# Kernel tuning notes

Measured on AMD Instinct MI355X. Metric: run time of the kernel, lower is better.

## Reference

```python
import jax, jax.numpy as jnp
import numpy as np

HEADS = 24
HEAD_DIM = 96
SPARSE_N = 4
ROPE_BASE = 10000.0


def _rope_cos_sin(pos, D):
    # pos: [L] int positions; D: per-axis rotary dim (even)
    inv_freq = 1.0 / (ROPE_BASE ** (jnp.arange(0, D, 2, dtype=jnp.float32) / D))
    f = pos.astype(jnp.float32)[:, None] * inv_freq[None, :]   # [L, D/2] (interp scale = 1)
    f = jnp.concatenate([f, f], axis=-1)                        # [L, D]
    return jnp.cos(f), jnp.sin(f)


def _rotate_half(x):
    x1, x2 = jnp.split(x, 2, axis=-1)
    return jnp.concatenate([-x2, x1], axis=-1)


def _apply_rope3d(tok, frame, height, width):
    # tok: [b, h, s, d]; RoPE3D splits head_dim into 3 equal chunks for (t, y, x)
    D = tok.shape[-1] // 3
    t = jnp.repeat(jnp.arange(frame), height * width)
    y = jnp.tile(jnp.repeat(jnp.arange(height), width), frame)
    x = jnp.tile(jnp.arange(width), frame * height)
    outs = []
    for i, pos in enumerate((t, y, x)):
        cos, sin = _rope_cos_sin(pos, D)                        # [s, D]
        part = tok[..., i * D:(i + 1) * D]
        outs.append(part * cos[None, None] + _rotate_half(part) * sin[None, None])
    return jnp.concatenate(outs, axis=-1)


def _sparse_1d(x, n):
    # 'b h (g k) d -> (k b) h g d' with pad so s % n*n == 0
    b, h, s, d = x.shape
    pad = (-s) % (n * n)
    if pad:
        x = jnp.pad(x, ((0, 0), (0, 0), (0, pad), (0, 0)))
    g = (s + pad) // n
    x = x.reshape(b, h, g, n, d)
    return jnp.transpose(x, (3, 0, 1, 2, 4)).reshape(n * b, h, g, d), pad


def _reverse_sparse_1d(x, n, s):
    # '(k b) h g d -> b h (g k) d' then crop to s tokens
    kb, h, g, d = x.shape
    b = kb // n
    x = x.reshape(n, b, h, g, d)
    x = jnp.transpose(x, (1, 2, 3, 0, 4)).reshape(b, h, g * n, d)
    return x[:, :, :s, :]


def setup_inputs() -> dict:
    key = jax.random.key(0)
    ks = jax.random.split(key, 5)
    dim = HEADS * HEAD_DIM
    b, f, hh, ww = 1, 8, 16, 32
    s = f * hh * ww
    inp = {
        "hidden_states": jax.random.normal(ks[0], (b, s, dim), dtype=jnp.float32),
        "wq": jax.random.normal(ks[1], (dim, dim), dtype=jnp.float32) * 0.02,
        "bq": jnp.zeros((dim,), jnp.float32),
        "wk": jax.random.normal(ks[2], (dim, dim), dtype=jnp.float32) * 0.02,
        "bk": jnp.zeros((dim,), jnp.float32),
        "wv": jax.random.normal(ks[3], (dim, dim), dtype=jnp.float32) * 0.02,
        "bv": jnp.zeros((dim,), jnp.float32),
        "wo": jax.random.normal(ks[4], (dim, dim), dtype=jnp.float32) * 0.02,
        "bo": jnp.zeros((dim,), jnp.float32),
        "frame": f, "height": hh, "width": ww,
    }
    return inp


def reference(hidden_states, wq, bq, wk, bk, wv, bv, wo, bo, frame, height, width):
    b, s, dim = hidden_states.shape
    assert s == frame * height * width

    def proj(w, bias):
        y = hidden_states @ w + bias                            # [b, s, dim]
        return jnp.transpose(y.reshape(b, s, HEADS, HEAD_DIM), (0, 2, 1, 3))  # [b, h, s, d]

    q = proj(wq, bq)
    k = proj(wk, bk)
    v = proj(wv, bv)

    # 3D rotary embedding on q, k (self-attention path)
    q = _apply_rope3d(q, frame, height, width)
    k = _apply_rope3d(k, frame, height, width)

    # sparse-1d grouping (sparse_group=False): strided token groups of size s/sparse_n
    q, _ = _sparse_1d(q, SPARSE_N)
    k, _ = _sparse_1d(k, SPARSE_N)
    v, _ = _sparse_1d(v, SPARSE_N)

    scale = 1.0 / jnp.sqrt(jnp.asarray(HEAD_DIM, jnp.float32))
    scores = jnp.einsum('bhqd,bhkd->bhqk', q, k) * scale        # [(n b), h, g, g]
    probs = jax.nn.softmax(scores, axis=-1)
    out = jnp.einsum('bhqk,bhkd->bhqd', probs, v)

    out = _reverse_sparse_1d(out, SPARSE_N, s)                   # [b, h, s, d]
    out = jnp.transpose(out, (0, 2, 1, 3)).reshape(b, s, dim)
    return out @ wo + bo
```

## Files before the change

### kernel.cpp

```cpp
#include <hip/hip_runtime.h>
#include <stdint.h>

#define S_TOK 4096
#define DIM   2304
#define NH    24
#define DH    96
#define GQ    1024
#define KDIM  2304

typedef unsigned short ushort_t;
typedef __attribute__((ext_vector_type(8))) short bf16x8;
typedef __attribute__((ext_vector_type(4))) float f32x4;

__device__ __forceinline__ ushort_t f2bf(float x) {
    union { float f; uint32_t u; } c; c.f = x;
    uint32_t u = c.u + 0x7FFFu + ((c.u >> 16) & 1u);
    return (ushort_t)(u >> 16);
}

#define GLDS(gp, lp) __builtin_amdgcn_global_load_lds( \
    (const __attribute__((address_space(1))) void*)(gp), \
    (__attribute__((address_space(3))) void*)(lp), 16, 0, 0)

__global__ __launch_bounds__(256) void cast_bf16_kernel(const float* __restrict__ in,
                                                        ushort_t* __restrict__ out, int n4) {
    int i = blockIdx.x * 256 + threadIdx.x;
    if (i >= n4) return;
    float4 v = ((const float4*)in)[i];
    ushort4 o;
    o.x = f2bf(v.x); o.y = f2bf(v.y); o.z = f2bf(v.z); o.w = f2bf(v.w);
    ((ushort4*)out)[i] = o;
}

__global__ __launch_bounds__(256) void wtrans_kernel(const float* __restrict__ W0,
                                                     const float* __restrict__ W1,
                                                     const float* __restrict__ W2,
                                                     const float* __restrict__ W3,
                                                     ushort_t* __restrict__ WT0, int dim) {
    __shared__ float tile[32][33];
    const int z = blockIdx.z;
    const float* W = (z == 0) ? W0 : (z == 1) ? W1 : (z == 2) ? W2 : W3;
    ushort_t* WT = WT0 + (size_t)z * dim * dim;
    const int bx = blockIdx.x * 32;
    const int by = blockIdx.y * 32;
    const int tx = threadIdx.x & 31, ty = threadIdx.x >> 5;
#pragma unroll
    for (int i = 0; i < 4; ++i)
        tile[ty + i*8][tx] = W[(size_t)(by + ty + i*8) * dim + bx + tx];
    __syncthreads();
#pragma unroll
    for (int i = 0; i < 4; ++i)
        WT[(size_t)(bx + ty + i*8) * dim + by + tx] = f2bf(tile[tx][ty + i*8]);
}

template<bool FINAL>
__global__ __launch_bounds__(512, 2) void gemm256(const ushort_t* __restrict__ A,
                                                  const ushort_t* __restrict__ Bt,
                                                  const float* __restrict__ bq,
                                                  const float* __restrict__ bk,
                                                  const float* __restrict__ bv,
                                                  ushort_t* __restrict__ Qb,
                                                  ushort_t* __restrict__ Kb,
                                                  ushort_t* __restrict__ Vtb,
                                                  float* __restrict__ Cf) {
    constexpr int K  = KDIM;
    constexpr int NT = K / 32;
    __shared__ ushort_t a_s[4 * 8192];
    __shared__ ushort_t b_s[4 * 8192];
    const int t = threadIdx.x, l = t & 63, w = t >> 6;
    const int wr = w >> 2, wc = w & 3, g = l >> 4, ln = l & 15;
    const int nwg = gridDim.x * gridDim.y;
    const int lin = blockIdx.y * gridDim.x + blockIdx.x;
    const int cpx = nwg >> 3;
    const int swz = (lin & 7) * cpx + (lin >> 3);
    const int bx = swz % gridDim.x, by = swz / gridDim.x;
    const int m0 = by * 256, n0 = bx * 256;

    const int swz_rd = (g ^ ((ln >> 1) & 3)) * 8;
    const int kc_src = (((t & 3) ^ ((t >> 3) & 3)) * 8);
    const int srow   = t >> 2;

    auto stageA = [&](int kt) {
        const int slot = kt & 3;
#pragma unroll
        for (int q = 0; q < 2; ++q)
            GLDS(A + (size_t)(m0 + q*128 + srow) * K + kt*32 + kc_src,
                 &a_s[slot*8192 + (q*512 + t) * 8]);
    };
    auto stageB = [&](int kt) {
        const int slot = kt & 3;
#pragma unroll
        for (int q = 0; q < 2; ++q)
            GLDS(Bt + (size_t)(n0 + q*128 + srow) * K + kt*32 + kc_src,
                 &b_s[slot*8192 + (q*512 + t) * 8]);
    };

    f32x4 acc[8][4] = {};

    stageA(0); stageB(0); stageA(1); stageB(1); stageA(2); stageB(2);
    asm volatile("s_waitcnt vmcnt(8)" ::: "memory");
    __builtin_amdgcn_s_barrier();

    for (int kt = 0; kt < NT; ++kt) {
        const int slot = kt & 3;
        bf16x8 bv4[4];
        {
            bf16x8 av[4];
#pragma unroll
            for (int j = 0; j < 4; ++j)
                bv4[j] = *(const bf16x8*)&b_s[slot*8192 + (wc*64 + j*16 + ln)*32 + swz_rd];
#pragma unroll
            for (int i = 0; i < 4; ++i)
                av[i] = *(const bf16x8*)&a_s[slot*8192 + (wr*128 + i*16 + ln)*32 + swz_rd];
            if (kt < NT - 3) stageA(kt + 3);
            __builtin_amdgcn_s_barrier();
            asm volatile("s_waitcnt lgkmcnt(0)" ::: "memory");
            __builtin_amdgcn_sched_barrier(0);
            __builtin_amdgcn_s_setprio(1);
#pragma unroll
            for (int i = 0; i < 4; ++i)
#pragma unroll
                for (int j = 0; j < 4; ++j)
                    acc[i][j] = __builtin_amdgcn_mfma_f32_16x16x32_bf16(av[i], bv4[j], acc[i][j], 0, 0, 0);
            __builtin_amdgcn_s_setprio(0);
        }
        {
            bf16x8 av[4];
#pragma unroll
            for (int i = 0; i < 4; ++i)
                av[i] = *(const bf16x8*)&a_s[slot*8192 + (wr*128 + 64 + i*16 + ln)*32 + swz_rd];
            if (kt < NT - 3) stageB(kt + 3);
            if (kt <= NT - 4)      asm volatile("s_waitcnt vmcnt(8)" ::: "memory");
            else if (kt == NT - 3) asm volatile("s_waitcnt vmcnt(4)" ::: "memory");
            else                   asm volatile("s_waitcnt vmcnt(0)" ::: "memory");
            __builtin_amdgcn_s_barrier();
            asm volatile("s_waitcnt lgkmcnt(0)" ::: "memory");
            __builtin_amdgcn_sched_barrier(0);
            __builtin_amdgcn_s_setprio(1);
#pragma unroll
            for (int i = 0; i < 4; ++i)
#pragma unroll
                for (int j = 0; j < 4; ++j)
                    acc[4 + i][j] = __builtin_amdgcn_mfma_f32_16x16x32_bf16(av[i], bv4[j], acc[4 + i][j], 0, 0, 0);
            __builtin_amdgcn_s_setprio(0);
        }
    }

    if constexpr (FINAL) {
        const float* bias = bq;
#pragma unroll
        for (int i = 0; i < 8; ++i) {
            int mb = m0 + wr*128 + i*16 + g*4;
#pragma unroll
            for (int j = 0; j < 4; ++j) {
                int n = n0 + wc*64 + j*16 + ln;
                float bb = bias[n];
#pragma unroll
                for (int r = 0; r < 4; ++r)
                    Cf[(size_t)(mb + r) * DIM + n] = acc[i][j][r] + bb;
            }
        }
    } else {
        const int mode = bx / 9;
        const int nb = (bx - mode * 9) * 256;
        const float* bias = (mode == 0) ? bq : (mode == 1) ? bk : bv;
        if (mode == 2) {
#pragma unroll
            for (int i = 0; i < 8; ++i) {
                int mb = m0 + wr*128 + i*16 + g*4;
                int q  = mb >> 2;
#pragma unroll
                for (int j = 0; j < 4; ++j) {
                    int nm = nb + wc*64 + j*16 + ln;
                    int hh = nm / DH, d = nm - hh * DH;
                    float bb = bias[nm];
#pragma unroll
                    for (int r = 0; r < 4; ++r)
                        Vtb[(size_t)(r * NH + hh) * (DH * GQ) + (size_t)d * GQ + q] =
                            f2bf(acc[i][j][r] + bb);
                }
            }
        } else {
            ushort_t* O = (mode == 0) ? Qb : Kb;
            const float scq = (mode == 0) ? 0.1020620726159658f : 1.0f;
#pragma unroll
            for (int i = 0; i < 8; ++i) {
                int mb = m0 + wr*128 + i*16 + g*4;
#pragma unroll
                for (int jp = 0; jp < 2; ++jp) {
                    int j  = jp * 2;
                    int n1 = nb + wc*64 + j*16 + ln;
                    int hh = n1 / DH, d1 = n1 - hh * DH;
                    int sec = d1 >> 5, f = d1 & 15;
                    float invf = __expf((float)f * -0.5756462732485114f);
                    float b1 = bias[n1], b2 = bias[n1 + 16];
#pragma unroll
                    for (int r = 0; r < 4; ++r) {
                        int m = mb + r;
                        int pos = (sec == 0) ? (m >> 9) : (sec == 1) ? ((m >> 5) & 15) : (m & 31);
                        float ang = (float)pos * invf;
                        float sn, cs;
                        __sincosf(ang, &sn, &cs);
                        float v1 = acc[i][j][r]     + b1;
                        float v2 = acc[i][j + 1][r] + b2;
                        size_t base = ((size_t)((m & 3) * NH + hh)) * (GQ * DH) + (size_t)(m >> 2) * DH;
                        O[base + d1]      = f2bf((v1 * cs - v2 * sn) * scq);
                        O[base + d1 + 16] = f2bf((v2 * cs + v1 * sn) * scq);
                    }
                }
            }
        }
    }
}

__global__ __launch_bounds__(256) void gemm128(const ushort_t* __restrict__ A,
                                               const ushort_t* __restrict__ Bt,
                                               const float* __restrict__ bias,
                                               float* __restrict__ C) {
    constexpr int K = KDIM;
    __shared__ ushort_t a_s[128 * 32];
    __shared__ ushort_t b_s[128 * 32];
    const int t = threadIdx.x;
    const int l = t & 63, w = t >> 6;
    const int wr = w >> 1, wc = w & 1;
    const int g = l >> 4, ln = l & 15;
    const int lin = blockIdx.y * gridDim.x + blockIdx.x;
    const int swz = (lin & 7) * 72 + (lin >> 3);
    const int bx = swz % 18, by = swz / 18;
    const int m0 = by * 128, n0 = bx * 128;

    const int swz_rd = (g ^ ((ln >> 1) & 3)) * 8;
    const int kc_src = (((t & 3) ^ ((t >> 3) & 3)) * 8);
    const int srow   = t >> 2;

    const ushort_t* Ab = A  + (size_t)(m0 + srow) * K + kc_src;
    const ushort_t* Bb = Bt + (size_t)(n0 + srow) * K + kc_src;
    ushort_t* a_d0 = a_s + t * 8;
    ushort_t* a_d1 = a_s + 2048 + t * 8;
    ushort_t* b_d0 = b_s + t * 8;
    ushort_t* b_d1 = b_s + 2048 + t * 8;
    const size_t rstep = (size_t)64 * K;

    f32x4 acc[4][4] = {};

    for (int k0 = 0; k0 < K; k0 += 32) {
        __syncthreads();
        GLDS(Ab + k0,         a_d0);
        GLDS(Ab + rstep + k0, a_d1);
        GLDS(Bb + k0,         b_d0);
        GLDS(Bb + rstep + k0, b_d1);
        __syncthreads();
        bf16x8 av[4], bv[4];
#pragma unroll
        for (int i = 0; i < 4; ++i)
            av[i] = *(const bf16x8*)&a_s[(wr*64 + i*16 + ln) * 32 + swz_rd];
#pragma unroll
        for (int j = 0; j < 4; ++j)
            bv[j] = *(const bf16x8*)&b_s[(wc*64 + j*16 + ln) * 32 + swz_rd];
#pragma unroll
        for (int i = 0; i < 4; ++i)
#pragma unroll
            for (int j = 0; j < 4; ++j)
                acc[i][j] = __builtin_amdgcn_mfma_f32_16x16x32_bf16(av[i], bv[j], acc[i][j], 0, 0, 0);
    }

#pragma unroll
    for (int i = 0; i < 4; ++i) {
        int mb = m0 + wr*64 + i*16 + g*4;
#pragma unroll
        for (int j = 0; j < 4; ++j) {
            int n = n0 + wc*64 + j*16 + ln;
            float bb = bias[n];
#pragma unroll
            for (int r = 0; r < 4; ++r)
                C[(size_t)(mb + r) * DIM + n] = acc[i][j][r] + bb;
        }
    }
}

__global__ __launch_bounds__(256, 3) void attn_kernel(const ushort_t* __restrict__ Qb,
                                                      const ushort_t* __restrict__ Kb,
                                                      const ushort_t* __restrict__ Vt,
                                                      ushort_t* __restrict__ ATT) {
    __shared__ ushort_t k_s[2][12 * 64 * 8];
    __shared__ ushort_t v_s[8 * 96 * 8];
    __shared__ ushort_t p_s[4 * 2 * 16 * 64];

    const int t = threadIdx.x, l = t & 63, w = t >> 6, g = l >> 4, ln = l & 15;
    const int lin  = blockIdx.x;
    const int swz  = (lin & 7) * 96 + (lin >> 3);
    const int inst = swz >> 3;
    const int qb0  = (swz & 7) * 128;
    const int n_idx = inst / NH, h = inst - n_idx * NH;
    const int swzp = (ln & 7) << 3;

    const ushort_t* Qi = Qb + (size_t)inst * (GQ * DH);
    const ushort_t* Ki = Kb + (size_t)inst * (GQ * DH);
    const ushort_t* Vi = Vt + (size_t)inst * (DH * GQ);

    auto stageK = [&](int kt, int b) {
#pragma unroll
        for (int it = 0; it < 3; ++it) {
            int P = t + it * 256;
            int c = P >> 6, key = P & 63;
            GLDS(Ki + (size_t)(kt * 64 + key) * DH + c * 8, &k_s[b][P * 8]);
        }
    };
    auto stageV = [&](int kt) {
#pragma unroll
        for (int it = 0; it < 3; ++it) {
            int P = t + it * 256;
            int c = P / 96, d = P - c * 96;
            GLDS(Vi + (size_t)d * GQ + kt * 64 + c * 8, &v_s[P * 8]);
        }
    };

    bf16x8 qf[2][3];
#pragma unroll
    for (int qt = 0; qt < 2; ++qt)
#pragma unroll
        for (int ks = 0; ks < 3; ++ks)
            qf[qt][ks] = *(const bf16x8*)(Qi + (size_t)(qb0 + w*32 + qt*16 + ln) * DH + ks*32 + g*8);

    float m_run[2], l_run[2];
#pragma unroll
    for (int qt = 0; qt < 2; ++qt) { m_run[qt] = -3.0e38f; l_run[qt] = 0.f; }
    f32x4 acc_o[2][6] = {};

    stageK(0, 0);
    stageV(0);
    __syncthreads();

    int cur = 0;
    for (int kt = 0; kt < 16; ++kt) {
        stageK((kt + 1) & 15, cur ^ 1);
        float al2[2];

        f32x4 sc[2][4] = {};
#pragma unroll
        for (int ct = 0; ct < 4; ++ct) {
            bf16x8 kf0 = *(const bf16x8*)&k_s[cur][((0*4 + g)*64 + ct*16 + ln) * 8];
            bf16x8 kf1 = *(const bf16x8*)&k_s[cur][((1*4 + g)*64 + ct*16 + ln) * 8];
            bf16x8 kf2 = *(const bf16x8*)&k_s[cur][((2*4 + g)*64 + ct*16 + ln) * 8];
#pragma unroll
            for (int qi = 0; qi < 2; ++qi) {
                sc[qi][ct] = __builtin_amdgcn_mfma_f32_16x16x32_bf16(kf0, qf[qi][0], sc[qi][ct], 0, 0, 0);
                sc[qi][ct] = __builtin_amdgcn_mfma_f32_16x16x32_bf16(kf1, qf[qi][1], sc[qi][ct], 0, 0, 0);
                sc[qi][ct] = __builtin_amdgcn_mfma_f32_16x16x32_bf16(kf2, qf[qi][2], sc[qi][ct], 0, 0, 0);
            }
        }
#pragma unroll
        for (int qi = 0; qi < 2; ++qi) {
            const int qt = qi;
            float mx = sc[qi][0][0];
#pragma unroll
            for (int ct = 0; ct < 4; ++ct)
#pragma unroll
                for (int r = 0; r < 4; ++r)
                    mx = fmaxf(mx, sc[qi][ct][r]);
            mx = fmaxf(mx, __shfl_xor(mx, 16, 64));
            mx = fmaxf(mx, __shfl_xor(mx, 32, 64));
            float mn = fmaxf(m_run[qt], mx);
            float al = __expf(m_run[qt] - mn);
            m_run[qt] = mn;
            float rs = 0.f;
            ushort_t pb[16];
#pragma unroll
            for (int ct = 0; ct < 4; ++ct)
#pragma unroll
                for (int r = 0; r < 4; ++r) {
                    float p = __expf(sc[qi][ct][r] - mn);
                    rs += p;
                    pb[ct*4 + r] = f2bf(p);
                }
            rs += __shfl_xor(rs, 16, 64);
            rs += __shfl_xor(rs, 32, 64);
            l_run[qt] = l_run[qt] * al + rs;
            al2[qt] = al;
            const int pbase = ((w*2 + qt)*16 + ln) * 64;
#pragma unroll
            for (int ct = 0; ct < 4; ++ct) {
                ushort4 pk;
                pk.x = pb[ct*4+0]; pk.y = pb[ct*4+1]; pk.z = pb[ct*4+2]; pk.w = pb[ct*4+3];
                *(ushort4*)&p_s[pbase + ((ct*16 + g*4) ^ swzp)] = pk;
            }
        }

#pragma unroll
        for (int qt = 0; qt < 2; ++qt)
#pragma unroll
            for (int r = 0; r < 4; ++r) {
                float a = __shfl(al2[qt], g*4 + r, 16);
#pragma unroll
                for (int dt = 0; dt < 6; ++dt)
                    acc_o[qt][dt][r] *= a;
            }

        asm volatile("s_waitcnt vmcnt(3)" ::: "memory");
        __builtin_amdgcn_s_barrier();
        __builtin_amdgcn_sched_barrier(0);
        asm volatile("s_waitcnt lgkmcnt(0)" ::: "memory");
        __builtin_amdgcn_sched_barrier(0);

#pragma unroll
        for (int kb = 0; kb < 2; ++kb) {
            bf16x8 pf2[2];
#pragma unroll
            for (int qt = 0; qt < 2; ++qt)
                pf2[qt] = *(const bf16x8*)&p_s[((w*2 + qt)*16 + ln)*64 + ((kb*32 + g*8) ^ swzp)];
#pragma unroll
            for (int dt = 0; dt < 6; ++dt) {
                bf16x8 vf = *(const bf16x8*)&v_s[((kb*4 + g)*96 + dt*16 + ln) * 8];
#pragma unroll
                for (int qt = 0; qt < 2; ++qt)
                    acc_o[qt][dt] = __builtin_amdgcn_mfma_f32_16x16x32_bf16(pf2[qt], vf, acc_o[qt][dt], 0, 0, 0);
            }
        }

        __syncthreads();
        if (kt < 15) stageV(kt + 1);
        cur ^= 1;
    }

#pragma unroll
    for (int qt = 0; qt < 2; ++qt) {
        float inv = 1.0f / l_run[qt];
#pragma unroll
        for (int r = 0; r < 4; ++r) {
            float iv = __shfl(inv, g*4 + r, 16);
            int gq = qb0 + w*32 + qt*16 + g*4 + r;
            size_t base = ((size_t)(gq * 4 + n_idx)) * DIM + h * DH;
#pragma unroll
            for (int dt = 0; dt < 6; ++dt)
                ATT[base + dt*16 + ln] = f2bf(acc_o[qt][dt][r] * iv);
        }
    }
}

extern "C" void kernel_launch(void* const* d_in, const int* in_sizes, int n_in,
                              void* d_out, int out_size, void* d_ws, size_t ws_size,
                              hipStream_t stream) {
    const float* hidden = (const float*)d_in[0];
    const float* wq = (const float*)d_in[1];
    const float* bq = (const float*)d_in[2];
    const float* wk = (const float*)d_in[3];
    const float* bk = (const float*)d_in[4];
    const float* wv = (const float*)d_in[5];
    const float* bv = (const float*)d_in[6];
    const float* wo = (const float*)d_in[7];
    const float* bo = (const float*)d_in[8];
    float* out = (float*)d_out;

    char* ws = (char*)d_ws;
    ushort_t* Xb  = (ushort_t*)ws;
    ushort_t* WTq = (ushort_t*)(ws + 18874368);
    ushort_t* WTk = WTq + (size_t)DIM * DIM;
    ushort_t* WTv = WTk + (size_t)DIM * DIM;
    ushort_t* WTo = WTv + (size_t)DIM * DIM;
    ushort_t* Qb  = WTo + (size_t)DIM * DIM;
    ushort_t* Kb  = Qb + (size_t)S_TOK * DIM;
    ushort_t* Vtb = Kb + (size_t)S_TOK * DIM;
    ushort_t* ATT = Vtb + (size_t)S_TOK * DIM;

    cast_bf16_kernel<<<dim3(9216), dim3(256), 0, stream>>>(hidden, Xb, (S_TOK * DIM) / 4);

    wtrans_kernel<<<dim3(72, 72, 4), 256, 0, stream>>>(wq, wk, wv, wo, WTq, DIM);

    gemm256<false><<<dim3(27, 16), 512, 0, stream>>>(Xb, WTq, bq, bk, bv, Qb, Kb, Vtb, nullptr);

    attn_kernel<<<dim3(768), 256, 0, stream>>>(Qb, Kb, Vtb, ATT);

    gemm128<<<dim3(18, 32), 256, 0, stream>>>(ATT, WTo, bo, out);
}
```

Measured before the change: 328.0 us.

## Double-buffer LDS in output-projection GEMM with prefetch-two-ahead pipeline

Converts the gemm128 main loop from a single LDS buffer with two barriers per k-step into a two-slot ring. Global-to-LDS loads are issued two tiles ahead, with explicit vmcnt waits and barriers, so memory latency overlaps with the MFMA work. It also raises wave priority around the MFMA block. LDS use doubles, which may reduce occupancy, and the hand-placed waitcnt and barrier ordering must stay correct to avoid races.

```diff
diff --git a/kernel.cpp b/kernel.cpp
--- a/kernel.cpp
+++ b/kernel.cpp
@@ -217,9 +217,10 @@
                                                const ushort_t* __restrict__ Bt,
                                                const float* __restrict__ bias,
                                                float* __restrict__ C) {
-    constexpr int K = KDIM;
-    __shared__ ushort_t a_s[128 * 32];
-    __shared__ ushort_t b_s[128 * 32];
+    constexpr int K  = KDIM;
+    constexpr int NT = K / 32;
+    __shared__ ushort_t a_s[2 * 4096];
+    __shared__ ushort_t b_s[2 * 4096];
     const int t = threadIdx.x;
     const int l = t & 63, w = t >> 6;
     const int wr = w >> 1, wc = w & 1;
@@ -235,33 +236,50 @@
 
     const ushort_t* Ab = A  + (size_t)(m0 + srow) * K + kc_src;
     const ushort_t* Bb = Bt + (size_t)(n0 + srow) * K + kc_src;
-    ushort_t* a_d0 = a_s + t * 8;
-    ushort_t* a_d1 = a_s + 2048 + t * 8;
-    ushort_t* b_d0 = b_s + t * 8;
-    ushort_t* b_d1 = b_s + 2048 + t * 8;
     const size_t rstep = (size_t)64 * K;
 
+    auto stage = [&](int kt) {
+        const int slot = kt & 1;
+        GLDS(Ab + kt*32,         &a_s[slot*4096 + t*8]);
+        GLDS(Ab + rstep + kt*32, &a_s[slot*4096 + 2048 + t*8]);
+        GLDS(Bb + kt*32,         &b_s[slot*4096 + t*8]);
+        GLDS(Bb + rstep + kt*32, &b_s[slot*4096 + 2048 + t*8]);
+    };
+
     f32x4 acc[4][4] = {};
 
-    for (int k0 = 0; k0 < K; k0 += 32) {
-        __syncthreads();
-        GLDS(Ab + k0,         a_d0);
-        GLDS(Ab + rstep + k0, a_d1);
-        GLDS(Bb + k0,         b_d0);
-        GLDS(Bb + rstep + k0, b_d1);
-        __syncthreads();
+    stage(0); stage(1);
+    asm volatile("s_waitcnt vmcnt(4)" ::: "memory");
+    __builtin_amdgcn_s_barrier();
+
+    for (int kt = 0; kt < NT; ++kt) {
+        const int slot = kt & 1;
         bf16x8 av[4], bv[4];
 #pragma unroll
         for (int i = 0; i < 4; ++i)
-            av[i] = *(const bf16x8*)&a_s[(wr*64 + i*16 + ln) * 32 + swz_rd];
+            av[i] = *(const bf16x8*)&a_s[slot*4096 + (wr*64 + i*16 + ln) * 32 + swz_rd];
 #pragma unroll
         for (int j = 0; j < 4; ++j)
-            bv[j] = *(const bf16x8*)&b_s[(wc*64 + j*16 + ln) * 32 + swz_rd];
+            bv[j] = *(const bf16x8*)&b_s[slot*4096 + (wc*64 + j*16 + ln) * 32 + swz_rd];
+        asm volatile("s_waitcnt lgkmcnt(0)" ::: "memory");
+        __builtin_amdgcn_sched_barrier(0);
+        __builtin_amdgcn_s_barrier();
+        if (kt < NT - 2) {
+            stage(kt + 2);
+            asm volatile("s_waitcnt vmcnt(4)" ::: "memory");
+        } else {
+            asm volatile("s_waitcnt vmcnt(0)" ::: "memory");
+        }
+        __builtin_amdgcn_sched_barrier(0);
+        __builtin_amdgcn_s_setprio(1);
 #pragma unroll
         for (int i = 0; i < 4; ++i)
 #pragma unroll
             for (int j = 0; j < 4; ++j)
                 acc[i][j] = __builtin_amdgcn_mfma_f32_16x16x32_bf16(av[i], bv[j], acc[i][j], 0, 0, 0);
+        __builtin_amdgcn_s_setprio(0);
+        __builtin_amdgcn_sched_barrier(0);
+        __builtin_amdgcn_s_barrier();
     }
 
 #pragma unroll
```

After: 327.9 us. Within noise of the previous version (-0.1%).
